# Optimization experiments

Measured on AMD Instinct MI355X. Metric: run time of the kernel, lower is better.

Reference implementation:

```python
import jax, jax.numpy as jnp
import numpy as np

# Config (matches init_kwargs)
S = 8            # num_seqs
LQ = 256         # query tokens per sequence (num_tokens = S*LQ = 2048)
SEQ = 2048       # kv seq_len per sequence
BLK = 16         # block size
NBLK_PER_SEQ = SEQ // BLK   # 128 = max_num_blocks_per_seq
NUM_BLKS = S * NBLK_PER_SEQ # 1024
HQ = 32          # num_query_heads
HKV = 8          # num_kv_heads
G = HQ // HKV    # queries per kv head (GQA group)
D = 128          # head_size
WINDOW = 1024    # sliding_window
SCALE = 1.0 / float(np.sqrt(D))


def setup_inputs() -> dict:
    key = jax.random.key(0)
    k1, k2, k3 = jax.random.split(key, 3)
    query = jax.random.normal(k1, (S * LQ, HQ, D), jnp.float32)
    key_cache = jax.random.normal(k2, (NUM_BLKS, BLK, HKV, D), jnp.float32)
    value_cache = jax.random.normal(k3, (NUM_BLKS, BLK, HKV, D), jnp.float32)
    # each sequence owns a contiguous run of blocks; all indices valid (>=0)
    block_tables = jnp.arange(NUM_BLKS, dtype=jnp.int32).reshape(S, NBLK_PER_SEQ)
    seq_lens = jnp.full((S,), SEQ, dtype=jnp.int32)
    query_start_len = (jnp.arange(S + 1, dtype=jnp.int32) * LQ)
    return dict(query=query, key_cache=key_cache, value_cache=value_cache,
                block_tables=block_tables, seq_lens=seq_lens,
                query_start_len=query_start_len)


def reference(query, key_cache, value_cache, block_tables, seq_lens, query_start_len):
    # query: [S*LQ, HQ, D] -> [S, LQ, HKV, G, D]
    q = query.reshape(S, LQ, HKV, G, D)
    # paged KV gather: [S, NBLK_PER_SEQ] -> [S, NBLK_PER_SEQ, BLK, HKV, D] -> [S, SEQ, HKV, D]
    K = key_cache[block_tables].reshape(S, SEQ, HKV, D)
    V = value_cache[block_tables].reshape(S, SEQ, HKV, D)
    # attention scores: [S, HKV, G, LQ, SEQ]
    scores = jnp.einsum('sqhgd,skhd->shgqk', q, K) * SCALE
    # causal + sliding-window mask over absolute positions
    ctx = SEQ - LQ  # context_len (same for all seqs here)
    qpos = ctx + jnp.arange(LQ)          # [LQ] absolute query positions
    kpos = jnp.arange(SEQ)               # [SEQ] absolute key positions
    valid = (kpos[None, :] <= qpos[:, None]) & \
            (qpos[:, None] - kpos[None, :] < WINDOW)   # [LQ, SEQ]
    neg_inf = jnp.asarray(-jnp.inf, scores.dtype)
    scores = jnp.where(valid[None, None, None, :, :], scores, neg_inf)
    probs = jax.nn.softmax(scores, axis=-1)
    # output: [S, LQ, HKV, G, D] -> [S*LQ, HQ, D]
    out = jnp.einsum('shgqk,skhd->sqhgd', probs, V)
    return out.reshape(S * LQ, HQ, D)
```

## Files before the change

### kernel.cpp

```cpp
#include <hip/hip_runtime.h>
#include <stdint.h>

typedef __attribute__((ext_vector_type(8))) short short8;
typedef __attribute__((ext_vector_type(4))) float floatx4;
typedef __attribute__((ext_vector_type(16))) float f32x16;
typedef __attribute__((ext_vector_type(4))) unsigned int uint4v;
typedef __attribute__((ext_vector_type(2))) unsigned int uint2v;

#define NSEQ 8
#define BLKSZ 16
#define NBLK_PER_SEQ 128
#define HQN 32
#define HKVN 8
#define GQ 4
#define HD 128
#define WINDOW 1024
#define QSCALE 0.12751744f

#define QB 32
#define KVB 64
#define KROW 136
#define VROW 72

#define MFMA32 __builtin_amdgcn_mfma_f32_32x32x16_bf16

static __device__ __forceinline__ unsigned int pack2bf(float lo, float hi) {
    unsigned int a = __builtin_bit_cast(unsigned int, lo) + 0x8000u;
    unsigned int b = __builtin_bit_cast(unsigned int, hi) + 0x8000u;
    return __builtin_amdgcn_perm(b, a, 0x07060302u);
}

static __device__ __forceinline__ float xhalf_max(float x) {
    return fmaxf(x, __shfl_xor(x, 32));
}

__global__ __launch_bounds__(256, 2)
void attn_fwd(const float* __restrict__ qg,
              const float* __restrict__ kg,
              const float* __restrict__ vg,
              const int* __restrict__ bt,
              const int* __restrict__ seqlens,
              const int* __restrict__ qsl,
              float* __restrict__ outg)
{
    __shared__ __align__(16) short Klds[KVB][KROW];
    __shared__ __align__(16) short Vt[2][HD][VROW];

    const int tid  = threadIdx.x;
    const int lane = tid & 63;
    const int wave = tid >> 6;
    const int l31  = lane & 31;
    const int hi   = lane >> 5;

    const int b  = blockIdx.x;
    const int h  = b & 7;
    const int qt = (b >> 3) & 7;
    const int s  = b >> 6;
    const int q0 = qt * QB;

    const int qstart = qsl[s];
    const int numq   = qsl[s + 1] - qstart;
    const int slen   = seqlens[s];
    const int ctx    = slen - numq;
    const int hq     = h * GQ + wave;

    short8 qf[8];
    {
        const float* qrow = qg + ((size_t)(qstart + q0 + l31) * HQN + hq) * HD;
        #pragma unroll
        for (int ks = 0; ks < 8; ++ks) {
            floatx4 f0 = *(const floatx4*)(qrow + ks * 16 + hi * 8);
            floatx4 f1 = *(const floatx4*)(qrow + ks * 16 + hi * 8 + 4);
            uint4v w;
            w[0] = pack2bf(f0[0] * QSCALE, f0[1] * QSCALE);
            w[1] = pack2bf(f0[2] * QSCALE, f0[3] * QSCALE);
            w[2] = pack2bf(f1[0] * QSCALE, f1[1] * QSCALE);
            w[3] = pack2bf(f1[2] * QSCALE, f1[3] * QSCALE);
            qf[ks] = __builtin_bit_cast(short8, w);
        }
    }

    f32x16 oacc[4];
    #pragma unroll
    for (int dblk = 0; dblk < 4; ++dblk)
        #pragma unroll
        for (int i = 0; i < 16; ++i)
            oacc[dblk][i] = 0.f;

    float mrun = -INFINITY;
    float lrun = 0.f;

    int lo = ctx + q0 - WINDOW + 1; if (lo < 0) lo = 0;
    int hiq = ctx + q0 + QB - 1;    if (hiq > slen - 1) hiq = slen - 1;
    const int t0 = lo / KVB, t1 = hiq / KVB;

    const int srow = tid >> 3;
    const int sd0  = (tid & 7) * 16;
    const int j4   = tid & 15;
    const int d0v  = (tid >> 4) * 8;

    floatx4 fk[8], fv[8];

#define LOAD_K_HALF(kv0_, p) {                                                       \
        const int kvp = (kv0_) + (p) * 32 + srow;                                    \
        const int blk = bt[s * NBLK_PER_SEQ + (kvp >> 4)];                           \
        const float* src = kg + (((size_t)blk * BLKSZ + (kvp & 15)) * HKVN + h) * HD + sd0; \
        fk[(p)*4+0] = *(const floatx4*)(src);                                        \
        fk[(p)*4+1] = *(const floatx4*)(src + 4);                                    \
        fk[(p)*4+2] = *(const floatx4*)(src + 8);                                    \
        fk[(p)*4+3] = *(const floatx4*)(src + 12);                                   \
    }
#define LOAD_V(kv0_) {                                                               \
        const int kvv = (kv0_) + 4 * j4;                                             \
        const int blkv = bt[s * NBLK_PER_SEQ + (kvv >> 4)];                          \
        const float* vsrc = vg + (((size_t)blkv * BLKSZ + (kvv & 15)) * HKVN + h) * HD + d0v; \
        fv[0] = *(const floatx4*)(vsrc);                                             \
        fv[4] = *(const floatx4*)(vsrc + 4);                                         \
        fv[1] = *(const floatx4*)(vsrc + 1024);                                      \
        fv[5] = *(const floatx4*)(vsrc + 1028);                                      \
        fv[2] = *(const floatx4*)(vsrc + 2048);                                      \
        fv[6] = *(const floatx4*)(vsrc + 2052);                                      \
        fv[3] = *(const floatx4*)(vsrc + 3072);                                      \
        fv[7] = *(const floatx4*)(vsrc + 3076);                                      \
    }
#define LOAD_TILE(kv0_) { LOAD_K_HALF(kv0_, 0); LOAD_K_HALF(kv0_, 1); LOAD_V(kv0_); }

    LOAD_TILE(t0 * KVB);

    for (int t = t0; t <= t1; ++t) {
        const int kv0 = t * KVB;
        const int vb  = t & 1;

        #pragma unroll
        for (int p = 0; p < 2; ++p) {
            const int row = p * 32 + srow;
            uint4v w;
            w[0] = pack2bf(fk[p*4+0][0], fk[p*4+0][1]);
            w[1] = pack2bf(fk[p*4+0][2], fk[p*4+0][3]);
            w[2] = pack2bf(fk[p*4+1][0], fk[p*4+1][1]);
            w[3] = pack2bf(fk[p*4+1][2], fk[p*4+1][3]);
            *(uint4v*)&Klds[row][sd0] = w;
            w[0] = pack2bf(fk[p*4+2][0], fk[p*4+2][1]);
            w[1] = pack2bf(fk[p*4+2][2], fk[p*4+2][3]);
            w[2] = pack2bf(fk[p*4+3][0], fk[p*4+3][1]);
            w[3] = pack2bf(fk[p*4+3][2], fk[p*4+3][3]);
            *(uint4v*)&Klds[row][sd0 + 8] = w;
        }
        #pragma unroll
        for (int d = 0; d < 8; ++d) {
            const float r0 = (d < 4) ? fv[0][d] : fv[4][d - 4];
            const float r1 = (d < 4) ? fv[1][d] : fv[5][d - 4];
            const float r2 = (d < 4) ? fv[2][d] : fv[6][d - 4];
            const float r3 = (d < 4) ? fv[3][d] : fv[7][d - 4];
            uint2v w;
            w[0] = pack2bf(r0, r1);
            w[1] = pack2bf(r2, r3);
            *(uint2v*)&Vt[vb][d0v + d][4 * j4] = w;
        }

        __syncthreads();

        f32x16 sacc0, sacc1;
        #pragma unroll
        for (int i = 0; i < 16; ++i) { sacc0[i] = 0.f; sacc1[i] = 0.f; }
        #pragma unroll
        for (int ks = 0; ks < 8; ++ks) {
            short8 kf0 = *(const short8*)&Klds[l31][ks * 16 + hi * 8];
            short8 kf1 = *(const short8*)&Klds[32 + l31][ks * 16 + hi * 8];
            sacc0 = MFMA32(kf0, qf[ks], sacc0, 0, 0, 0);
            sacc1 = MFMA32(kf1, qf[ks], sacc1, 0, 0, 0);
        }

        __syncthreads();

        if (t < t1) LOAD_TILE(kv0 + KVB);

        const bool interior = (kv0 >= ctx + q0 - (WINDOW - QB)) &&
                              (kv0 + KVB - 1 <= ctx + q0);
        const int qpos = ctx + q0 + l31;
        float p2[2][16];
        #pragma unroll
        for (int m2 = 0; m2 < 2; ++m2) {
            #pragma unroll
            for (int r = 0; r < 16; ++r) {
                float x = (m2 == 0) ? sacc0[r] : sacc1[r];
                if (!interior) {
                    const int kpos = kv0 + m2 * 32 + (r & 3) + 4 * hi + 8 * (r >> 2);
                    const bool valid = (kpos <= qpos) && (qpos - kpos < WINDOW);
                    x = valid ? x : -INFINITY;
                }
                p2[m2][r] = x;
            }
        }
        float tmax[16];
        #pragma unroll
        for (int r = 0; r < 16; ++r) tmax[r] = fmaxf(p2[0][r], p2[1][r]);
        #pragma unroll
        for (int s2 = 8; s2 > 0; s2 >>= 1)
            #pragma unroll
            for (int r = 0; r < 8; ++r)
                if (r < s2) tmax[r] = fmaxf(tmax[r], tmax[r + s2]);
        float rmax = xhalf_max(tmax[0]);

        const float mold = mrun;
        const bool defer = __all(rmax <= mold + 11.0f);
        const float mnew = defer ? mold : fmaxf(mold, rmax);
        const float alpha = defer ? 1.0f
            : ((mold == -INFINITY) ? ((mnew == -INFINITY) ? 1.0f : 0.0f)
                                   : exp2f(mold - mnew));
        const bool dead = (mnew == -INFINITY);
        #pragma unroll
        for (int m2 = 0; m2 < 2; ++m2)
            #pragma unroll
            for (int r = 0; r < 16; ++r)
                p2[m2][r] = dead ? 0.f : exp2f(p2[m2][r] - mnew);
        float ts[16];
        #pragma unroll
        for (int r = 0; r < 16; ++r) ts[r] = p2[0][r] + p2[1][r];
        #pragma unroll
        for (int s2 = 8; s2 > 0; s2 >>= 1)
            #pragma unroll
            for (int r = 0; r < 8; ++r)
                if (r < s2) ts[r] = ts[r] + ts[r + s2];
        lrun = lrun * alpha + ts[0];
        mrun = mnew;
        if (!defer) {
            #pragma unroll
            for (int dblk = 0; dblk < 4; ++dblk)
                oacc[dblk] = oacc[dblk] * alpha;
        }

        short8 pb[2][2];
        #pragma unroll
        for (int m2 = 0; m2 < 2; ++m2) {
            unsigned int c0 = pack2bf(p2[m2][0],  p2[m2][1]);
            unsigned int c1 = pack2bf(p2[m2][2],  p2[m2][3]);
            unsigned int c2 = pack2bf(p2[m2][4],  p2[m2][5]);
            unsigned int c3 = pack2bf(p2[m2][6],  p2[m2][7]);
            unsigned int c4 = pack2bf(p2[m2][8],  p2[m2][9]);
            unsigned int c5 = pack2bf(p2[m2][10], p2[m2][11]);
            unsigned int c6 = pack2bf(p2[m2][12], p2[m2][13]);
            unsigned int c7 = pack2bf(p2[m2][14], p2[m2][15]);
            unsigned int s0 = hi ? c0 : c2;
            unsigned int s1 = hi ? c1 : c3;
            unsigned int s2 = hi ? c4 : c6;
            unsigned int s3 = hi ? c5 : c7;
            unsigned int r0 = (unsigned int)__shfl_xor((int)s0, 32);
            unsigned int r1 = (unsigned int)__shfl_xor((int)s1, 32);
            unsigned int r2 = (unsigned int)__shfl_xor((int)s2, 32);
            unsigned int r3 = (unsigned int)__shfl_xor((int)s3, 32);
            uint4v u0, u1;
            u0[0] = hi ? r0 : c0;
            u0[1] = hi ? r1 : c1;
            u0[2] = hi ? c2 : r0;
            u0[3] = hi ? c3 : r1;
            u1[0] = hi ? r2 : c4;
            u1[1] = hi ? r3 : c5;
            u1[2] = hi ? c6 : r2;
            u1[3] = hi ? c7 : r3;
            pb[m2][0] = __builtin_bit_cast(short8, u0);
            pb[m2][1] = __builtin_bit_cast(short8, u1);
        }

        #pragma unroll
        for (int m2 = 0; m2 < 2; ++m2) {
            #pragma unroll
            for (int dblk = 0; dblk < 4; ++dblk) {
                short8 vf0 = *(const short8*)&Vt[vb][dblk * 32 + l31][m2 * 32 + hi * 8];
                short8 vf1 = *(const short8*)&Vt[vb][dblk * 32 + l31][m2 * 32 + 16 + hi * 8];
                oacc[dblk] = MFMA32(vf0, pb[m2][0], oacc[dblk], 0, 0, 0);
                oacc[dblk] = MFMA32(vf1, pb[m2][1], oacc[dblk], 0, 0, 0);
            }
        }
    }
#undef LOAD_TILE
#undef LOAD_V
#undef LOAD_K_HALF

    {
        const float ltot = lrun + __shfl_xor(lrun, 32);
        const float inv = 1.0f / ltot;
        float* orow = outg + ((size_t)(qstart + q0 + l31) * HQN + hq) * HD;
        #pragma unroll
        for (int dblk = 0; dblk < 4; ++dblk) {
            #pragma unroll
            for (int rq = 0; rq < 4; ++rq) {
                floatx4 o;
                o[0] = oacc[dblk][4 * rq + 0] * inv;
                o[1] = oacc[dblk][4 * rq + 1] * inv;
                o[2] = oacc[dblk][4 * rq + 2] * inv;
                o[3] = oacc[dblk][4 * rq + 3] * inv;
                *(floatx4*)(orow + dblk * 32 + 8 * rq + 4 * hi) = o;
            }
        }
    }
}

extern "C" void kernel_launch(void* const* d_in, const int* in_sizes, int n_in,
                              void* d_out, int out_size, void* d_ws, size_t ws_size,
                              hipStream_t stream) {
    const float* q  = (const float*)d_in[0];
    const float* k  = (const float*)d_in[1];
    const float* v  = (const float*)d_in[2];
    const int* btp  = (const int*)d_in[3];
    const int* sl   = (const int*)d_in[4];
    const int* qs   = (const int*)d_in[5];
    float* out      = (float*)d_out;

    attn_fwd<<<dim3(NSEQ * HKVN * 8), 256, 0, stream>>>(q, k, v, btp, sl, qs, out);
}
```

Before: 79.37 us.

## Software-pipeline PV MFMA of previous tile behind current tile's softmax

Moves the P·V matrix multiply for tile t-1 so it runs after the QK MFMAs of tile t, using the already double-buffered V tile and carrying the packed probabilities and rescale factor across iterations. This lets the softmax math and shuffles of the current tile overlap with matrix-core work, and it merges two barriers into one at the end of the loop. A final PV step after the loop drains the pipeline. It costs extra registers for the carried probability fragments. The first iteration multiplies zero probabilities against an unwritten V buffer, so uninitialized LDS holding NaN bit patterns could corrupt the output.

```diff
diff --git a/kernel.cpp b/kernel.cpp
--- a/kernel.cpp
+++ b/kernel.cpp
@@ -126,6 +126,17 @@
 #define LOAD_TILE(kv0_) { LOAD_K_HALF(kv0_, 0); LOAD_K_HALF(kv0_, 1); LOAD_V(kv0_); }
 
     LOAD_TILE(t0 * KVB);
+
+    short8 pbPrev[2][2];
+    {
+        uint4v z; z[0] = 0u; z[1] = 0u; z[2] = 0u; z[3] = 0u;
+        pbPrev[0][0] = __builtin_bit_cast(short8, z);
+        pbPrev[0][1] = __builtin_bit_cast(short8, z);
+        pbPrev[1][0] = __builtin_bit_cast(short8, z);
+        pbPrev[1][1] = __builtin_bit_cast(short8, z);
+    }
+    float alphaPrev = 1.0f;
+    bool  rescPrev  = false;
 
     for (int t = t0; t <= t1; ++t) {
         const int kv0 = t * KVB;
@@ -171,9 +182,26 @@
             sacc1 = MFMA32(kf1, qf[ks], sacc1, 0, 0, 0);
         }
 
-        __syncthreads();
-
         if (t < t1) LOAD_TILE(kv0 + KVB);
+
+        if (rescPrev) {
+            #pragma unroll
+            for (int dblk = 0; dblk < 4; ++dblk)
+                oacc[dblk] = oacc[dblk] * alphaPrev;
+        }
+        {
+            const int vbp = vb ^ 1;
+            #pragma unroll
+            for (int m2 = 0; m2 < 2; ++m2) {
+                #pragma unroll
+                for (int dblk = 0; dblk < 4; ++dblk) {
+                    short8 vf0 = *(const short8*)&Vt[vbp][dblk * 32 + l31][m2 * 32 + hi * 8];
+                    short8 vf1 = *(const short8*)&Vt[vbp][dblk * 32 + l31][m2 * 32 + 16 + hi * 8];
+                    oacc[dblk] = MFMA32(vf0, pbPrev[m2][0], oacc[dblk], 0, 0, 0);
+                    oacc[dblk] = MFMA32(vf1, pbPrev[m2][1], oacc[dblk], 0, 0, 0);
+                }
+            }
+        }
 
         const bool interior = (kv0 >= ctx + q0 - (WINDOW - QB)) &&
                               (kv0 + KVB - 1 <= ctx + q0);
@@ -224,13 +252,7 @@
                 if (r < s2) ts[r] = ts[r] + ts[r + s2];
         lrun = lrun * alpha + ts[0];
         mrun = mnew;
-        if (!defer) {
-            #pragma unroll
-            for (int dblk = 0; dblk < 4; ++dblk)
-                oacc[dblk] = oacc[dblk] * alpha;
-        }
-
-        short8 pb[2][2];
+
         #pragma unroll
         for (int m2 = 0; m2 < 2; ++m2) {
             unsigned int c0 = pack2bf(p2[m2][0],  p2[m2][1]);
@@ -258,26 +280,35 @@
             u1[1] = hi ? r3 : c5;
             u1[2] = hi ? c6 : r2;
             u1[3] = hi ? c7 : r3;
-            pb[m2][0] = __builtin_bit_cast(short8, u0);
-            pb[m2][1] = __builtin_bit_cast(short8, u1);
-        }
-
-        #pragma unroll
-        for (int m2 = 0; m2 < 2; ++m2) {
-            #pragma unroll
-            for (int dblk = 0; dblk < 4; ++dblk) {
-                short8 vf0 = *(const short8*)&Vt[vb][dblk * 32 + l31][m2 * 32 + hi * 8];
-                short8 vf1 = *(const short8*)&Vt[vb][dblk * 32 + l31][m2 * 32 + 16 + hi * 8];
-                oacc[dblk] = MFMA32(vf0, pb[m2][0], oacc[dblk], 0, 0, 0);
-                oacc[dblk] = MFMA32(vf1, pb[m2][1], oacc[dblk], 0, 0, 0);
-            }
-        }
+            pbPrev[m2][0] = __builtin_bit_cast(short8, u0);
+            pbPrev[m2][1] = __builtin_bit_cast(short8, u1);
+        }
+        alphaPrev = alpha;
+        rescPrev  = !defer;
+
+        __syncthreads();
     }
 #undef LOAD_TILE
 #undef LOAD_V
 #undef LOAD_K_HALF
 
     {
+        if (rescPrev) {
+            #pragma unroll
+            for (int dblk = 0; dblk < 4; ++dblk)
+                oacc[dblk] = oacc[dblk] * alphaPrev;
+        }
+        const int vbl = t1 & 1;
+        #pragma unroll
+        for (int m2 = 0; m2 < 2; ++m2) {
+            #pragma unroll
+            for (int dblk = 0; dblk < 4; ++dblk) {
+                short8 vf0 = *(const short8*)&Vt[vbl][dblk * 32 + l31][m2 * 32 + hi * 8];
+                short8 vf1 = *(const short8*)&Vt[vbl][dblk * 32 + l31][m2 * 32 + 16 + hi * 8];
+                oacc[dblk] = MFMA32(vf0, pbPrev[m2][0], oacc[dblk], 0, 0, 0);
+                oacc[dblk] = MFMA32(vf1, pbPrev[m2][1], oacc[dblk], 0, 0, 0);
+            }
+        }
         const float ltot = lrun + __shfl_xor(lrun, 32);
         const float inv = 1.0f / ltot;
         float* orow = outg + ((size_t)(qstart + q0 + l31) * HQN + hq) * HD;
```

Result: slower. 81.33 us (+2.5%).

## Split GQA heads across two workgroups, halve KV tile, double-buffer K in LDS

Applied to the files above, without the earlier changes.

Each workgroup now runs 2 waves covering half the query heads of a KV group, so the grid is twice as large with 128 threads per block. The KV tile shrinks from 64 to 32 rows, and K gets a double buffer in LDS, which removes the second barrier per tile. The goal is more parallelism and occupancy, plus less sync stall per iteration. In exchange, every K/V tile is loaded and converted twice (once per head-pair workgroup), and there are twice as many loop iterations with smaller MFMA batches.

```diff
diff --git a/kernel.cpp b/kernel.cpp
--- a/kernel.cpp
+++ b/kernel.cpp
@@ -18,9 +18,9 @@
 #define QSCALE 0.12751744f
 
 #define QB 32
-#define KVB 64
+#define KVB 32
 #define KROW 136
-#define VROW 72
+#define VROW 40
 
 #define MFMA32 __builtin_amdgcn_mfma_f32_32x32x16_bf16
 
@@ -34,7 +34,7 @@
     return fmaxf(x, __shfl_xor(x, 32));
 }
 
-__global__ __launch_bounds__(256, 2)
+__global__ __launch_bounds__(128, 2)
 void attn_fwd(const float* __restrict__ qg,
               const float* __restrict__ kg,
               const float* __restrict__ vg,
@@ -43,7 +43,7 @@
               const int* __restrict__ qsl,
               float* __restrict__ outg)
 {
-    __shared__ __align__(16) short Klds[KVB][KROW];
+    __shared__ __align__(16) short Klds[2][KVB][KROW];
     __shared__ __align__(16) short Vt[2][HD][VROW];
 
     const int tid  = threadIdx.x;
@@ -55,14 +55,15 @@
     const int b  = blockIdx.x;
     const int h  = b & 7;
     const int qt = (b >> 3) & 7;
-    const int s  = b >> 6;
+    const int hp = (b >> 6) & 1;
+    const int s  = b >> 7;
     const int q0 = qt * QB;
 
     const int qstart = qsl[s];
     const int numq   = qsl[s + 1] - qstart;
     const int slen   = seqlens[s];
     const int ctx    = slen - numq;
-    const int hq     = h * GQ + wave;
+    const int hq     = h * GQ + hp * 2 + wave;
 
     short8 qf[8];
     {
@@ -94,21 +95,21 @@
     int hiq = ctx + q0 + QB - 1;    if (hiq > slen - 1) hiq = slen - 1;
     const int t0 = lo / KVB, t1 = hiq / KVB;
 
-    const int srow = tid >> 3;
-    const int sd0  = (tid & 7) * 16;
-    const int j4   = tid & 15;
-    const int d0v  = (tid >> 4) * 8;
+    const int srow = tid >> 2;
+    const int sd0  = (tid & 3) * 32;
+    const int j4   = tid & 7;
+    const int d0v  = (tid >> 3) * 8;
 
     floatx4 fk[8], fv[8];
 
-#define LOAD_K_HALF(kv0_, p) {                                                       \
-        const int kvp = (kv0_) + (p) * 32 + srow;                                    \
+#define LOAD_K(kv0_) {                                                               \
+        const int kvp = (kv0_) + srow;                                               \
         const int blk = bt[s * NBLK_PER_SEQ + (kvp >> 4)];                           \
         const float* src = kg + (((size_t)blk * BLKSZ + (kvp & 15)) * HKVN + h) * HD + sd0; \
-        fk[(p)*4+0] = *(const floatx4*)(src);                                        \
-        fk[(p)*4+1] = *(const floatx4*)(src + 4);                                    \
-        fk[(p)*4+2] = *(const floatx4*)(src + 8);                                    \
-        fk[(p)*4+3] = *(const floatx4*)(src + 12);                                   \
+        fk[0] = *(const floatx4*)(src);        fk[1] = *(const floatx4*)(src + 4);   \
+        fk[2] = *(const floatx4*)(src + 8);    fk[3] = *(const floatx4*)(src + 12);  \
+        fk[4] = *(const floatx4*)(src + 16);   fk[5] = *(const floatx4*)(src + 20);  \
+        fk[6] = *(const floatx4*)(src + 24);   fk[7] = *(const floatx4*)(src + 28);  \
     }
 #define LOAD_V(kv0_) {                                                               \
         const int kvv = (kv0_) + 4 * j4;                                             \
@@ -123,7 +124,7 @@
         fv[3] = *(const floatx4*)(vsrc + 3072);                                      \
         fv[7] = *(const floatx4*)(vsrc + 3076);                                      \
     }
-#define LOAD_TILE(kv0_) { LOAD_K_HALF(kv0_, 0); LOAD_K_HALF(kv0_, 1); LOAD_V(kv0_); }
+#define LOAD_TILE(kv0_) { LOAD_K(kv0_); LOAD_V(kv0_); }
 
     LOAD_TILE(t0 * KVB);
 
@@ -131,20 +132,20 @@
         const int kv0 = t * KVB;
         const int vb  = t & 1;
 
-        #pragma unroll
-        for (int p = 0; p < 2; ++p) {
-            const int row = p * 32 + srow;
+        {
             uint4v w;
-            w[0] = pack2bf(fk[p*4+0][0], fk[p*4+0][1]);
-            w[1] = pack2bf(fk[p*4+0][2], fk[p*4+0][3]);
-            w[2] = pack2bf(fk[p*4+1][0], fk[p*4+1][1]);
-            w[3] = pack2bf(fk[p*4+1][2], fk[p*4+1][3]);
-            *(uint4v*)&Klds[row][sd0] = w;
-            w[0] = pack2bf(fk[p*4+2][0], fk[p*4+2][1]);
-            w[1] = pack2bf(fk[p*4+2][2], fk[p*4+2][3]);
-            w[2] = pack2bf(fk[p*4+3][0], fk[p*4+3][1]);
-            w[3] = pack2bf(fk[p*4+3][2], fk[p*4+3][3]);
-            *(uint4v*)&Klds[row][sd0 + 8] = w;
+            w[0] = pack2bf(fk[0][0], fk[0][1]); w[1] = pack2bf(fk[0][2], fk[0][3]);
+            w[2] = pack2bf(fk[1][0], fk[1][1]); w[3] = pack2bf(fk[1][2], fk[1][3]);
+            *(uint4v*)&Klds[vb][srow][sd0] = w;
+            w[0] = pack2bf(fk[2][0], fk[2][1]); w[1] = pack2bf(fk[2][2], fk[2][3]);
+            w[2] = pack2bf(fk[3][0], fk[3][1]); w[3] = pack2bf(fk[3][2], fk[3][3]);
+            *(uint4v*)&Klds[vb][srow][sd0 + 8] = w;
+            w[0] = pack2bf(fk[4][0], fk[4][1]); w[1] = pack2bf(fk[4][2], fk[4][3]);
+            w[2] = pack2bf(fk[5][0], fk[5][1]); w[3] = pack2bf(fk[5][2], fk[5][3]);
+            *(uint4v*)&Klds[vb][srow][sd0 + 16] = w;
+            w[0] = pack2bf(fk[6][0], fk[6][1]); w[1] = pack2bf(fk[6][2], fk[6][3]);
+            w[2] = pack2bf(fk[7][0], fk[7][1]); w[3] = pack2bf(fk[7][2], fk[7][3]);
+            *(uint4v*)&Klds[vb][srow][sd0 + 24] = w;
         }
         #pragma unroll
         for (int d = 0; d < 8; ++d) {
@@ -160,45 +161,38 @@
 
         __syncthreads();
 
-        f32x16 sacc0, sacc1;
-        #pragma unroll
-        for (int i = 0; i < 16; ++i) { sacc0[i] = 0.f; sacc1[i] = 0.f; }
+        f32x16 sacc;
+        #pragma unroll
+        for (int i = 0; i < 16; ++i) sacc[i] = 0.f;
         #pragma unroll
         for (int ks = 0; ks < 8; ++ks) {
-            short8 kf0 = *(const short8*)&Klds[l31][ks * 16 + hi * 8];
-            short8 kf1 = *(const short8*)&Klds[32 + l31][ks * 16 + hi * 8];
-            sacc0 = MFMA32(kf0, qf[ks], sacc0, 0, 0, 0);
-            sacc1 = MFMA32(kf1, qf[ks], sacc1, 0, 0, 0);
-        }
-
-        __syncthreads();
+            short8 kf = *(const short8*)&Klds[vb][l31][ks * 16 + hi * 8];
+            sacc = MFMA32(kf, qf[ks], sacc, 0, 0, 0);
+        }
 
         if (t < t1) LOAD_TILE(kv0 + KVB);
 
         const bool interior = (kv0 >= ctx + q0 - (WINDOW - QB)) &&
                               (kv0 + KVB - 1 <= ctx + q0);
         const int qpos = ctx + q0 + l31;
-        float p2[2][16];
-        #pragma unroll
-        for (int m2 = 0; m2 < 2; ++m2) {
-            #pragma unroll
-            for (int r = 0; r < 16; ++r) {
-                float x = (m2 == 0) ? sacc0[r] : sacc1[r];
-                if (!interior) {
-                    const int kpos = kv0 + m2 * 32 + (r & 3) + 4 * hi + 8 * (r >> 2);
-                    const bool valid = (kpos <= qpos) && (qpos - kpos < WINDOW);
-                    x = valid ? x : -INFINITY;
-                }
-                p2[m2][r] = x;
+        float p[16];
+        #pragma unroll
+        for (int r = 0; r < 16; ++r) {
+            float x = sacc[r];
+            if (!interior) {
+                const int kpos = kv0 + (r & 3) + 4 * hi + 8 * (r >> 2);
+                const bool valid = (kpos <= qpos) && (qpos - kpos < WINDOW);
+                x = valid ? x : -INFINITY;
             }
-        }
-        float tmax[16];
-        #pragma unroll
-        for (int r = 0; r < 16; ++r) tmax[r] = fmaxf(p2[0][r], p2[1][r]);
-        #pragma unroll
-        for (int s2 = 8; s2 > 0; s2 >>= 1)
-            #pragma unroll
-            for (int r = 0; r < 8; ++r)
+            p[r] = x;
+        }
+        float tmax[8];
+        #pragma unroll
+        for (int r = 0; r < 8; ++r) tmax[r] = fmaxf(p[r], p[r + 8]);
+        #pragma unroll
+        for (int s2 = 4; s2 > 0; s2 >>= 1)
+            #pragma unroll
+            for (int r = 0; r < 4; ++r)
                 if (r < s2) tmax[r] = fmaxf(tmax[r], tmax[r + s2]);
         float rmax = xhalf_max(tmax[0]);
 
@@ -210,17 +204,15 @@
                                    : exp2f(mold - mnew));
         const bool dead = (mnew == -INFINITY);
         #pragma unroll
-        for (int m2 = 0; m2 < 2; ++m2)
-            #pragma unroll
-            for (int r = 0; r < 16; ++r)
-                p2[m2][r] = dead ? 0.f : exp2f(p2[m2][r] - mnew);
-        float ts[16];
-        #pragma unroll
-        for (int r = 0; r < 16; ++r) ts[r] = p2[0][r] + p2[1][r];
-        #pragma unroll
-        for (int s2 = 8; s2 > 0; s2 >>= 1)
-            #pragma unroll
-            for (int r = 0; r < 8; ++r)
+        for (int r = 0; r < 16; ++r)
+            p[r] = dead ? 0.f : exp2f(p[r] - mnew);
+        float ts[8];
+        #pragma unroll
+        for (int r = 0; r < 8; ++r) ts[r] = p[r] + p[r + 8];
+        #pragma unroll
+        for (int s2 = 4; s2 > 0; s2 >>= 1)
+            #pragma unroll
+            for (int r = 0; r < 4; ++r)
                 if (r < s2) ts[r] = ts[r] + ts[r + s2];
         lrun = lrun * alpha + ts[0];
         mrun = mnew;
@@ -230,17 +222,16 @@
                 oacc[dblk] = oacc[dblk] * alpha;
         }
 
-        short8 pb[2][2];
-        #pragma unroll
-        for (int m2 = 0; m2 < 2; ++m2) {
-            unsigned int c0 = pack2bf(p2[m2][0],  p2[m2][1]);
-            unsigned int c1 = pack2bf(p2[m2][2],  p2[m2][3]);
-            unsigned int c2 = pack2bf(p2[m2][4],  p2[m2][5]);
-            unsigned int c3 = pack2bf(p2[m2][6],  p2[m2][7]);
-            unsigned int c4 = pack2bf(p2[m2][8],  p2[m2][9]);
-            unsigned int c5 = pack2bf(p2[m2][10], p2[m2][11]);
-            unsigned int c6 = pack2bf(p2[m2][12], p2[m2][13]);
-            unsigned int c7 = pack2bf(p2[m2][14], p2[m2][15]);
+        short8 pb0, pb1;
+        {
+            unsigned int c0 = pack2bf(p[0],  p[1]);
+            unsigned int c1 = pack2bf(p[2],  p[3]);
+            unsigned int c2 = pack2bf(p[4],  p[5]);
+            unsigned int c3 = pack2bf(p[6],  p[7]);
+            unsigned int c4 = pack2bf(p[8],  p[9]);
+            unsigned int c5 = pack2bf(p[10], p[11]);
+            unsigned int c6 = pack2bf(p[12], p[13]);
+            unsigned int c7 = pack2bf(p[14], p[15]);
             unsigned int s0 = hi ? c0 : c2;
             unsigned int s1 = hi ? c1 : c3;
             unsigned int s2 = hi ? c4 : c6;
@@ -258,24 +249,21 @@
             u1[1] = hi ? r3 : c5;
             u1[2] = hi ? c6 : r2;
             u1[3] = hi ? c7 : r3;
-            pb[m2][0] = __builtin_bit_cast(short8, u0);
-            pb[m2][1] = __builtin_bit_cast(short8, u1);
-        }
-
-        #pragma unroll
-        for (int m2 = 0; m2 < 2; ++m2) {
-            #pragma unroll
-            for (int dblk = 0; dblk < 4; ++dblk) {
-                short8 vf0 = *(const short8*)&Vt[vb][dblk * 32 + l31][m2 * 32 + hi * 8];
-                short8 vf1 = *(const short8*)&Vt[vb][dblk * 32 + l31][m2 * 32 + 16 + hi * 8];
-                oacc[dblk] = MFMA32(vf0, pb[m2][0], oacc[dblk], 0, 0, 0);
-                oacc[dblk] = MFMA32(vf1, pb[m2][1], oacc[dblk], 0, 0, 0);
-            }
+            pb0 = __builtin_bit_cast(short8, u0);
+            pb1 = __builtin_bit_cast(short8, u1);
+        }
+
+        #pragma unroll
+        for (int dblk = 0; dblk < 4; ++dblk) {
+            short8 vf0 = *(const short8*)&Vt[vb][dblk * 32 + l31][hi * 8];
+            short8 vf1 = *(const short8*)&Vt[vb][dblk * 32 + l31][16 + hi * 8];
+            oacc[dblk] = MFMA32(vf0, pb0, oacc[dblk], 0, 0, 0);
+            oacc[dblk] = MFMA32(vf1, pb1, oacc[dblk], 0, 0, 0);
         }
     }
 #undef LOAD_TILE
 #undef LOAD_V
-#undef LOAD_K_HALF
+#undef LOAD_K
 
     {
         const float ltot = lrun + __shfl_xor(lrun, 32);
@@ -307,5 +295,5 @@
     const int* qs   = (const int*)d_in[5];
     float* out      = (float*)d_out;
 
-    attn_fwd<<<dim3(NSEQ * HKVN * 8), 256, 0, stream>>>(q, k, v, btp, sl, qs, out);
-}
+    attn_fwd<<<dim3(NSEQ * HKVN * 8 * 2), 128, 0, stream>>>(q, k, v, btp, sl, qs, out);
+}
```

New measurement: 140.0 us. 1.76x slower.

## Share each KV tile across two query sub-tiles with 512-thread blocks

Applied to the files above, without the earlier changes.

Doubles the query rows per block from 32 to 64 using 8 waves, with two groups of 4 waves each covering a 32-row query sub-tile. Each K/V tile loaded into LDS now serves twice as many queries, halving global KV traffic and conversion work per query. Each thread also loads half as much K/V data per tile. In exchange the grid shrinks from 512 to 256 blocks and the KV range per block widens slightly, so some tiles are loaded and masked for sub-tiles that do not need them. Larger blocks also raise register pressure under the launch bound.

```diff
diff --git a/kernel.cpp b/kernel.cpp
--- a/kernel.cpp
+++ b/kernel.cpp
@@ -17,7 +17,8 @@
 #define WINDOW 1024
 #define QSCALE 0.12751744f
 
-#define QB 32
+#define QBB 64
+#define QBW 32
 #define KVB 64
 #define KROW 136
 #define VROW 72
@@ -34,7 +35,7 @@
     return fmaxf(x, __shfl_xor(x, 32));
 }
 
-__global__ __launch_bounds__(256, 2)
+__global__ __launch_bounds__(512, 2)
 void attn_fwd(const float* __restrict__ qg,
               const float* __restrict__ kg,
               const float* __restrict__ vg,
@@ -49,24 +50,27 @@
     const int tid  = threadIdx.x;
     const int lane = tid & 63;
     const int wave = tid >> 6;
+    const int hw   = wave & 3;
+    const int qs2  = wave >> 2;
     const int l31  = lane & 31;
     const int hi   = lane >> 5;
 
     const int b  = blockIdx.x;
     const int h  = b & 7;
-    const int qt = (b >> 3) & 7;
-    const int s  = b >> 6;
-    const int q0 = qt * QB;
+    const int qt = (b >> 3) & 3;
+    const int s  = b >> 5;
+    const int q0 = qt * QBB;
+    const int qw0 = q0 + qs2 * QBW;
 
     const int qstart = qsl[s];
     const int numq   = qsl[s + 1] - qstart;
     const int slen   = seqlens[s];
     const int ctx    = slen - numq;
-    const int hq     = h * GQ + wave;
+    const int hq     = h * GQ + hw;
 
     short8 qf[8];
     {
-        const float* qrow = qg + ((size_t)(qstart + q0 + l31) * HQN + hq) * HD;
+        const float* qrow = qg + ((size_t)(qstart + qw0 + l31) * HQN + hq) * HD;
         #pragma unroll
         for (int ks = 0; ks < 8; ++ks) {
             floatx4 f0 = *(const floatx4*)(qrow + ks * 16 + hi * 8);
@@ -91,39 +95,35 @@
     float lrun = 0.f;
 
     int lo = ctx + q0 - WINDOW + 1; if (lo < 0) lo = 0;
-    int hiq = ctx + q0 + QB - 1;    if (hiq > slen - 1) hiq = slen - 1;
+    int hiq = ctx + q0 + QBB - 1;   if (hiq > slen - 1) hiq = slen - 1;
     const int t0 = lo / KVB, t1 = hiq / KVB;
 
     const int srow = tid >> 3;
     const int sd0  = (tid & 7) * 16;
     const int j4   = tid & 15;
-    const int d0v  = (tid >> 4) * 8;
-
-    floatx4 fk[8], fv[8];
-
-#define LOAD_K_HALF(kv0_, p) {                                                       \
-        const int kvp = (kv0_) + (p) * 32 + srow;                                    \
+    const int d0v  = (tid >> 4) * 4;
+
+    floatx4 fk[4], fv[4];
+
+#define LOAD_K(kv0_) {                                                               \
+        const int kvp = (kv0_) + srow;                                               \
         const int blk = bt[s * NBLK_PER_SEQ + (kvp >> 4)];                           \
         const float* src = kg + (((size_t)blk * BLKSZ + (kvp & 15)) * HKVN + h) * HD + sd0; \
-        fk[(p)*4+0] = *(const floatx4*)(src);                                        \
-        fk[(p)*4+1] = *(const floatx4*)(src + 4);                                    \
-        fk[(p)*4+2] = *(const floatx4*)(src + 8);                                    \
-        fk[(p)*4+3] = *(const floatx4*)(src + 12);                                   \
+        fk[0] = *(const floatx4*)(src);                                              \
+        fk[1] = *(const floatx4*)(src + 4);                                          \
+        fk[2] = *(const floatx4*)(src + 8);                                          \
+        fk[3] = *(const floatx4*)(src + 12);                                         \
     }
 #define LOAD_V(kv0_) {                                                               \
         const int kvv = (kv0_) + 4 * j4;                                             \
         const int blkv = bt[s * NBLK_PER_SEQ + (kvv >> 4)];                          \
         const float* vsrc = vg + (((size_t)blkv * BLKSZ + (kvv & 15)) * HKVN + h) * HD + d0v; \
         fv[0] = *(const floatx4*)(vsrc);                                             \
-        fv[4] = *(const floatx4*)(vsrc + 4);                                         \
         fv[1] = *(const floatx4*)(vsrc + 1024);                                      \
-        fv[5] = *(const floatx4*)(vsrc + 1028);                                      \
         fv[2] = *(const floatx4*)(vsrc + 2048);                                      \
-        fv[6] = *(const floatx4*)(vsrc + 2052);                                      \
         fv[3] = *(const floatx4*)(vsrc + 3072);                                      \
-        fv[7] = *(const floatx4*)(vsrc + 3076);                                      \
-    }
-#define LOAD_TILE(kv0_) { LOAD_K_HALF(kv0_, 0); LOAD_K_HALF(kv0_, 1); LOAD_V(kv0_); }
+    }
+#define LOAD_TILE(kv0_) { LOAD_K(kv0_); LOAD_V(kv0_); }
 
     LOAD_TILE(t0 * KVB);
 
@@ -131,30 +131,20 @@
         const int kv0 = t * KVB;
         const int vb  = t & 1;
 
-        #pragma unroll
-        for (int p = 0; p < 2; ++p) {
-            const int row = p * 32 + srow;
+        {
             uint4v w;
-            w[0] = pack2bf(fk[p*4+0][0], fk[p*4+0][1]);
-            w[1] = pack2bf(fk[p*4+0][2], fk[p*4+0][3]);
-            w[2] = pack2bf(fk[p*4+1][0], fk[p*4+1][1]);
-            w[3] = pack2bf(fk[p*4+1][2], fk[p*4+1][3]);
-            *(uint4v*)&Klds[row][sd0] = w;
-            w[0] = pack2bf(fk[p*4+2][0], fk[p*4+2][1]);
-            w[1] = pack2bf(fk[p*4+2][2], fk[p*4+2][3]);
-            w[2] = pack2bf(fk[p*4+3][0], fk[p*4+3][1]);
-            w[3] = pack2bf(fk[p*4+3][2], fk[p*4+3][3]);
-            *(uint4v*)&Klds[row][sd0 + 8] = w;
-        }
-        #pragma unroll
-        for (int d = 0; d < 8; ++d) {
-            const float r0 = (d < 4) ? fv[0][d] : fv[4][d - 4];
-            const float r1 = (d < 4) ? fv[1][d] : fv[5][d - 4];
-            const float r2 = (d < 4) ? fv[2][d] : fv[6][d - 4];
-            const float r3 = (d < 4) ? fv[3][d] : fv[7][d - 4];
+            w[0] = pack2bf(fk[0][0], fk[0][1]); w[1] = pack2bf(fk[0][2], fk[0][3]);
+            w[2] = pack2bf(fk[1][0], fk[1][1]); w[3] = pack2bf(fk[1][2], fk[1][3]);
+            *(uint4v*)&Klds[srow][sd0] = w;
+            w[0] = pack2bf(fk[2][0], fk[2][1]); w[1] = pack2bf(fk[2][2], fk[2][3]);
+            w[2] = pack2bf(fk[3][0], fk[3][1]); w[3] = pack2bf(fk[3][2], fk[3][3]);
+            *(uint4v*)&Klds[srow][sd0 + 8] = w;
+        }
+        #pragma unroll
+        for (int d = 0; d < 4; ++d) {
             uint2v w;
-            w[0] = pack2bf(r0, r1);
-            w[1] = pack2bf(r2, r3);
+            w[0] = pack2bf(fv[0][d], fv[1][d]);
+            w[1] = pack2bf(fv[2][d], fv[3][d]);
             *(uint2v*)&Vt[vb][d0v + d][4 * j4] = w;
         }
 
@@ -175,9 +165,9 @@
 
         if (t < t1) LOAD_TILE(kv0 + KVB);
 
-        const bool interior = (kv0 >= ctx + q0 - (WINDOW - QB)) &&
-                              (kv0 + KVB - 1 <= ctx + q0);
-        const int qpos = ctx + q0 + l31;
+        const bool interior = (kv0 >= ctx + qw0 - (WINDOW - QBW)) &&
+                              (kv0 + KVB - 1 <= ctx + qw0);
+        const int qpos = ctx + qw0 + l31;
         float p2[2][16];
         #pragma unroll
         for (int m2 = 0; m2 < 2; ++m2) {
@@ -275,12 +265,12 @@
     }
 #undef LOAD_TILE
 #undef LOAD_V
-#undef LOAD_K_HALF
+#undef LOAD_K
 
     {
         const float ltot = lrun + __shfl_xor(lrun, 32);
         const float inv = 1.0f / ltot;
-        float* orow = outg + ((size_t)(qstart + q0 + l31) * HQN + hq) * HD;
+        float* orow = outg + ((size_t)(qstart + qw0 + l31) * HQN + hq) * HD;
         #pragma unroll
         for (int dblk = 0; dblk < 4; ++dblk) {
             #pragma unroll
@@ -307,5 +297,5 @@
     const int* qs   = (const int*)d_in[5];
     float* out      = (float*)d_out;
 
-    attn_fwd<<<dim3(NSEQ * HKVN * 8), 256, 0, stream>>>(q, k, v, btp, sl, qs, out);
+    attn_fwd<<<dim3(NSEQ * HKVN * 4), 512, 0, stream>>>(q, k, v, btp, sl, qs, out);
 }
```

Result: no change. 80.91 us (+1.9%).
